# Performance work log

Hardware: AMD Instinct MI355X
Metric: run time of the kernel (lower is better)

## Reference

```python
import jax, jax.numpy as jnp
import numpy as np

B, S, D, H = 2, 2048, 1024, 16
HD = D // H


def setup_inputs() -> dict:
    key = jax.random.key(0)
    ks = jax.random.split(key, 8)
    scale = 1.0 / np.sqrt(D)
    return {
        "x": jax.random.normal(ks[0], (B, S, D), dtype=jnp.float32),
        "y": jax.random.normal(ks[1], (B, S, D), dtype=jnp.float32),
        "gamma": jnp.ones((D,), jnp.float32),
        "beta": jnp.zeros((D,), jnp.float32),
        "in_proj_w": jax.random.uniform(ks[2], (3 * D, D), jnp.float32, -scale, scale),
        "in_proj_b": jnp.zeros((3 * D,), jnp.float32),
        "out_w": jax.random.uniform(ks[3], (D, D), jnp.float32, -scale, scale),
        "out_b": jnp.zeros((D,), jnp.float32),
    }


def _layer_norm(x, gamma, beta, eps=1e-5):
    mu = jnp.mean(x, axis=-1, keepdims=True)
    var = jnp.mean((x - mu) ** 2, axis=-1, keepdims=True)
    return (x - mu) * jax.lax.rsqrt(var + eps) * gamma + beta


def reference(x, y, gamma, beta, in_proj_w, in_proj_b, out_w, out_b):
    # Pre-LN (note: y is unused by the original forward; q=k=v=norm(x))
    xn = _layer_norm(x, gamma, beta)
    # combined QKV projection, PyTorch convention: xn @ W^T + b
    qkv = jnp.einsum("bsd,ed->bse", xn, in_proj_w) + in_proj_b  # (B,S,3D)
    q, k, v = jnp.split(qkv, 3, axis=-1)
    # (B,H,S,HD)
    q = q.reshape(B, S, H, HD).transpose(0, 2, 1, 3)
    k = k.reshape(B, S, H, HD).transpose(0, 2, 1, 3)
    v = v.reshape(B, S, H, HD).transpose(0, 2, 1, 3)
    scores = jnp.einsum("bhqd,bhkd->bhqk", q, k) / np.sqrt(HD)
    attn = jax.nn.softmax(scores, axis=-1)  # (B,H,S,S)
    ctx = jnp.einsum("bhqk,bhkd->bhqd", attn, v)
    ctx = ctx.transpose(0, 2, 1, 3).reshape(B, S, D)
    out = jnp.einsum("bsd,ed->bse", ctx, out_w) + out_b
    # dropout p=0.0 -> identity; residual
    out = out + x
    # average_attn_weights=True default in PyTorch
    attn_w = jnp.mean(attn, axis=1)  # (B,S,S)
    return out, attn_w
```

## Files before the change

### kernel.cpp

```cpp
#include <hip/hip_runtime.h>
#include <hip/hip_bf16.h>

#define Bb 2
#define Ss 2048
#define Dd 1024
#define Hh 16
#define HDd 64
#define Mm (Bb*Ss)
#define N3 (3*Dd)

typedef __attribute__((ext_vector_type(8))) __bf16 bf16x8;
typedef __attribute__((ext_vector_type(4))) float f32x4;
typedef __attribute__((ext_vector_type(16))) float f32x16;
typedef __attribute__((ext_vector_type(8))) short short8;

__device__ __forceinline__ unsigned short f2b(float f) {
  unsigned int u = __float_as_uint(f);
  return (unsigned short)((u + 0x7fffu + ((u >> 16) & 1u)) >> 16);
}

__device__ __forceinline__ f32x4 mfma16(bf16x8 a, bf16x8 b, f32x4 c) {
  return __builtin_amdgcn_mfma_f32_16x16x32_bf16(a, b, c, 0, 0, 0);
}
__device__ __forceinline__ f32x16 mfma32(bf16x8 a, bf16x8 b, f32x16 c) {
  return __builtin_amdgcn_mfma_f32_32x32x16_bf16(a, b, c, 0, 0, 0);
}
__device__ __forceinline__ unsigned cvtpk(float lo, float hi) {
  unsigned r; asm("v_cvt_pk_bf16_f32 %0, %1, %2" : "=v"(r) : "v"(lo), "v"(hi)); return r;
}
__device__ __forceinline__ float fexp2(float x) {
  float r; asm("v_exp_f32 %0, %1" : "=v"(r) : "v"(x)); return r;
}
__device__ __forceinline__ void gload16(const unsigned short* g, unsigned short* l) {
  __builtin_amdgcn_global_load_lds((const __attribute__((address_space(1))) void*)g,
                                   (__attribute__((address_space(3))) void*)l, 16, 0, 0);
}

__global__ __launch_bounds__(256) void ln_kernel(const float* __restrict__ x,
                                                 const float* __restrict__ gamma,
                                                 const float* __restrict__ beta,
                                                 unsigned short* __restrict__ xn) {
  int row = blockIdx.x;
  const float* xr = x + (size_t)row * Dd;
  int t = threadIdx.x;
  float4 v = ((const float4*)xr)[t];
  float s  = v.x + v.y + v.z + v.w;
  float ss = v.x*v.x + v.y*v.y + v.z*v.z + v.w*v.w;
  for (int m = 1; m < 64; m <<= 1) { s += __shfl_xor(s, m, 64); ss += __shfl_xor(ss, m, 64); }
  __shared__ float rs[4], rss[4];
  int w = t >> 6;
  if ((t & 63) == 0) { rs[w] = s; rss[w] = ss; }
  __syncthreads();
  s  = rs[0] + rs[1] + rs[2] + rs[3];
  ss = rss[0] + rss[1] + rss[2] + rss[3];
  float mu   = s * (1.0f / Dd);
  float var  = ss * (1.0f / Dd) - mu * mu;
  float rstd = rsqrtf(var + 1e-5f);
  float4 g  = ((const float4*)gamma)[t];
  float4 be = ((const float4*)beta)[t];
  ushort4 o;
  o.x = f2b((v.x - mu) * rstd * g.x + be.x);
  o.y = f2b((v.y - mu) * rstd * g.y + be.y);
  o.z = f2b((v.z - mu) * rstd * g.z + be.z);
  o.w = f2b((v.w - mu) * rstd * g.w + be.w);
  ((ushort4*)(xn + (size_t)row * Dd))[t] = o;
}

__global__ __launch_bounds__(256) void castw_kernel(const float* __restrict__ w,
                                                    unsigned short* __restrict__ o, int n4) {
  for (int i = blockIdx.x * 256 + threadIdx.x; i < n4; i += gridDim.x * 256) {
    float4 v = ((const float4*)w)[i];
    ushort4 u; u.x = f2b(v.x); u.y = f2b(v.y); u.z = f2b(v.z); u.w = f2b(v.w);
    ((ushort4*)o)[i] = u;
  }
}

__global__ __launch_bounds__(256) void qkv_gemm_kernel(
    const unsigned short* __restrict__ A, const unsigned short* __restrict__ Bw,
    const float* __restrict__ bias,
    unsigned short* __restrict__ qb, unsigned short* __restrict__ kb,
    unsigned short* __restrict__ vtb) {
  __shared__ __align__(16) unsigned short As[64][64];
  __shared__ __align__(16) unsigned short Bs[128][64];
  const int t = threadIdx.x, l = t & 63, w = t >> 6;
  const int wr = w >> 1, wc = w & 1;
  const int lin = blockIdx.x;
  const int swz = (lin & 7) * 192 + (lin >> 3);
  const int mb = (swz & 63) * 64, nb = (swz >> 6) * 128;
  const int sc8 = ((l & 7) ^ ((l >> 3) & 7)) * 8;
  f32x4 acc[2][4];
  for (int i = 0; i < 2; i++) for (int j = 0; j < 4; j++) acc[i][j] = f32x4{0.f,0.f,0.f,0.f};
  for (int kt = 0; kt < 1024; kt += 64) {
    __syncthreads();
#pragma unroll
    for (int j = 0; j < 2; ++j) {
      int rbase = w*16 + j*8;
      gload16(&A[(size_t)(mb + rbase + (l >> 3))*1024 + kt + sc8], &As[rbase][0]);
    }
#pragma unroll
    for (int j = 0; j < 4; ++j) {
      int rbase = w*32 + j*8;
      gload16(&Bw[(size_t)(nb + rbase + (l >> 3))*1024 + kt + sc8], &Bs[rbase][0]);
    }
    __syncthreads();
#pragma unroll
    for (int ks = 0; ks < 2; ++ks) {
      bf16x8 af[2], bfr[4];
      const int g = ks*4 + (l >> 4);
#pragma unroll
      for (int i = 0; i < 2; i++) {
        int row = wr*32 + i*16 + (l & 15);
        af[i] = *(const bf16x8*)&As[row][(g ^ (row & 7))*8];
      }
#pragma unroll
      for (int j = 0; j < 4; j++) {
        int row = wc*64 + j*16 + (l & 15);
        bfr[j] = *(const bf16x8*)&Bs[row][(g ^ (row & 7))*8];
      }
#pragma unroll
      for (int i = 0; i < 2; i++)
#pragma unroll
        for (int j = 0; j < 4; j++)
          acc[i][j] = mfma16(af[i], bfr[j], acc[i][j]);
    }
  }
  const int rbase = (l >> 4) * 4;
#pragma unroll
  for (int i = 0; i < 2; i++) {
#pragma unroll
    for (int j = 0; j < 4; j++) {
      int ncol = nb + wc*64 + j*16 + (l & 15);
      int which = ncol >> 10, d = ncol & 1023, h = d >> 6, hd = d & 63;
      float bv = bias[ncol];
      int mrow0 = mb + wr*32 + i*16 + rbase;
      int b = mrow0 >> 11, s0 = mrow0 & 2047;
      if (which == 2) {
        ushort4 u;
        u.x = f2b(acc[i][j][0] + bv); u.y = f2b(acc[i][j][1] + bv);
        u.z = f2b(acc[i][j][2] + bv); u.w = f2b(acc[i][j][3] + bv);
        *(ushort4*)&vtb[((size_t)(b*Hh + h)*HDd + hd)*Ss + s0] = u;
      } else {
        unsigned short* dst = (which == 0) ? qb : kb;
        float sc = (which == 0) ? 0.18033688f : 1.0f;
#pragma unroll
        for (int r = 0; r < 4; r++)
          dst[((size_t)(b*Hh + h)*Ss + s0 + r)*HDd + hd] = f2b((acc[i][j][r] + bv) * sc);
      }
    }
  }
}

__global__ __launch_bounds__(512) void ctx_kernel(const unsigned short* __restrict__ q,
                                                  const unsigned short* __restrict__ k,
                                                  const unsigned short* __restrict__ vt,
                                                  float* __restrict__ linv,
                                                  unsigned short* __restrict__ ctxb) {
  const int bh = blockIdx.x, qt = blockIdx.y;
  const int b = bh >> 4, h = bh & 15;
  const unsigned short* qp  = q  + (size_t)bh * Ss * HDd;
  const unsigned short* kp  = k  + (size_t)bh * Ss * HDd;
  const unsigned short* vtp = vt + (size_t)bh * HDd * Ss;
  const int t = threadIdx.x, l = t & 63, w = t >> 6;
  const int wq = w & 3, wk = w >> 2;
  const int l31 = l & 31, hi = l >> 5;
  __shared__ __align__(16) unsigned short Ks[2][2][64][64];
  __shared__ __align__(16) unsigned short Vs[2][2][64][64];
  __shared__ float ls[8][32];
  const int qbase = qt*128 + wq*32;
  const int sc8 = ((l & 7) ^ ((l >> 3) & 7)) * 8;
  const int kofs = wk * 1024;
  bf16x8 qfr[4];
#pragma unroll
  for (int c = 0; c < 4; ++c)
    qfr[c] = *(const bf16x8*)&qp[(size_t)(qbase + l31)*HDd + c*16 + hi*8];
#pragma unroll
  for (int j = 0; j < 2; ++j) {
    int rbase = wq*16 + j*8;
    int row = rbase + (l >> 3);
    gload16(&kp [(size_t)(kofs + row)*HDd + sc8], &Ks[wk][0][rbase][0]);
    gload16(&vtp[(size_t)row*Ss + kofs + sc8],    &Vs[wk][0][rbase][0]);
  }
  __syncthreads();

  f32x16 cacc[2];
#pragma unroll
  for (int dj = 0; dj < 2; ++dj)
#pragma unroll
    for (int r = 0; r < 16; ++r) cacc[dj][r] = 0.f;
  float lsum = 0.f;

  for (int it = 0; it < 16; ++it) {
    const int cur = it & 1;
    if (it < 15) {
      int kt = kofs + (it + 1) * 64;
#pragma unroll
      for (int j = 0; j < 2; ++j) {
        int rbase = wq*16 + j*8;
        int row = rbase + (l >> 3);
        gload16(&kp [(size_t)(kt + row)*HDd + sc8], &Ks[wk][cur^1][rbase][0]);
        gload16(&vtp[(size_t)row*Ss + kt + sc8],    &Vs[wk][cur^1][rbase][0]);
      }
    }
#pragma unroll
    for (int kj = 0; kj < 2; ++kj) {
      f32x16 sacc;
#pragma unroll
      for (int r = 0; r < 16; ++r) sacc[r] = 0.f;
      __builtin_amdgcn_s_setprio(1);
#pragma unroll
      for (int c = 0; c < 4; ++c) {
        int R = kj*32 + l31;
        int s = 2*c + hi;
        bf16x8 kf = *(const bf16x8*)&Ks[wk][cur][R][(s ^ (R & 7))*8];
        sacc = mfma32(kf, qfr[c], sacc);
      }
      __builtin_amdgcn_s_setprio(0);
      float p[16];
#pragma unroll
      for (int r = 0; r < 16; ++r) { p[r] = fexp2(sacc[r]); lsum += p[r]; }
      unsigned xa = cvtpk(p[0],p[1]),   xb = cvtpk(p[4],p[5]);
      unsigned ya = cvtpk(p[2],p[3]),   yb = cvtpk(p[6],p[7]);
      unsigned za = cvtpk(p[8],p[9]),   zb = cvtpk(p[12],p[13]);
      unsigned wa = cvtpk(p[10],p[11]), wb = cvtpk(p[14],p[15]);
      asm volatile("v_permlane32_swap_b32 %0, %1" : "+v"(xa), "+v"(xb));
      asm volatile("v_permlane32_swap_b32 %0, %1" : "+v"(ya), "+v"(yb));
      asm volatile("v_permlane32_swap_b32 %0, %1" : "+v"(za), "+v"(zb));
      asm volatile("v_permlane32_swap_b32 %0, %1" : "+v"(wa), "+v"(wb));
      union { unsigned u[4]; bf16x8 v; } f0, f1;
      f0.u[0]=xa; f0.u[1]=ya; f0.u[2]=xb; f0.u[3]=yb;
      f1.u[0]=za; f1.u[1]=wa; f1.u[2]=zb; f1.u[3]=wb;
      __builtin_amdgcn_s_setprio(1);
#pragma unroll
      for (int kc = 0; kc < 2; ++kc) {
        bf16x8 pa = kc ? f1.v : f0.v;
#pragma unroll
        for (int dj = 0; dj < 2; ++dj) {
          int Rv = dj*32 + l31;
          int s = 4*kj + 2*kc + hi;
          bf16x8 vb = *(const bf16x8*)&Vs[wk][cur][Rv][(s ^ (Rv & 7))*8];
          cacc[dj] = mfma32(pa, vb, cacc[dj]);
        }
      }
      __builtin_amdgcn_s_setprio(0);
    }
    __syncthreads();
  }
  lsum += __shfl_xor(lsum, 32, 64);
  if (l < 32) ls[w][l] = lsum;
  float* scr = (float*)&Ks[0][0][0][0];
  if (wk == 1) {
#pragma unroll
    for (int dj = 0; dj < 2; ++dj)
#pragma unroll
      for (int r = 0; r < 16; ++r)
        scr[((wq*2 + dj)*16 + r)*64 + l] = cacc[dj][r];
  }
  __syncthreads();
  if (wk == 0) {
#pragma unroll
    for (int dj = 0; dj < 2; ++dj)
#pragma unroll
      for (int r = 0; r < 16; ++r)
        cacc[dj][r] += scr[((wq*2 + dj)*16 + r)*64 + l];
    if (l < 32) {
      float li = 1.0f / (ls[w][l] + ls[w + 4][l]);
      ls[w][l] = li;
      linv[(size_t)bh*Ss + qbase + l] = li;
    }
    float li4[4][4];
#pragma unroll
    for (int g = 0; g < 4; ++g) {
      f32x4 v4 = *(const f32x4*)&ls[w][8*g + 4*hi];
#pragma unroll
      for (int j = 0; j < 4; ++j) li4[g][j] = v4[j];
    }
#pragma unroll
    for (int dj = 0; dj < 2; ++dj) {
      int d = h*64 + dj*32 + l31;
#pragma unroll
      for (int r = 0; r < 16; ++r) {
        int qq = qbase + (r & 3) + 8*(r >> 2) + 4*hi;
        ctxb[((size_t)b*Ss + qq)*Dd + d] = f2b(cacc[dj][r] * li4[r >> 2][r & 3]);
      }
    }
  }
}

__global__ __launch_bounds__(256) void attnw_kernel(const unsigned short* __restrict__ q,
                                                    const unsigned short* __restrict__ k,
                                                    const float* __restrict__ linv,
                                                    float* __restrict__ attw) {
  const int lin = blockIdx.x;
  const int xcd = lin & 7, j0 = lin >> 3;
  const int ktile = (xcd & 3)*8 + (j0 & 7);
  const int qt    = (xcd >> 2)*8 + ((j0 >> 3) & 7);
  const int b     = j0 >> 6;
  const int t = threadIdx.x, l = t & 63, w = t >> 6;
  const int l31 = l & 31, hi = l >> 5;
  __shared__ union __align__(16) {
    struct { unsigned short qbuf[128][64]; unsigned short kbuf[64][64]; } g;
    float ps[128][68];
  } L;
  const int qbase = qt*128 + w*32;
  const int qrow = qbase + l31;
  const int sc8 = ((l & 7) ^ ((l >> 3) & 7)) * 8;

  float psum[2][16];
#pragma unroll
  for (int kj = 0; kj < 2; ++kj)
#pragma unroll
    for (int r = 0; r < 16; ++r) psum[kj][r] = 0.f;

#pragma unroll 1
  for (int h = 0; h < 16; ++h) {
    __syncthreads();
    const unsigned short* qp = q + ((size_t)(b*Hh + h)*Ss + (size_t)qt*128)*HDd;
    const unsigned short* kp = k + ((size_t)(b*Hh + h)*Ss + (size_t)ktile*64)*HDd;
#pragma unroll
    for (int j = 0; j < 4; ++j) {
      int rbase = w*32 + j*8;
      gload16(&qp[(size_t)(rbase + (l >> 3))*HDd + sc8], &L.g.qbuf[rbase][0]);
    }
#pragma unroll
    for (int j = 0; j < 2; ++j) {
      int rbase = w*16 + j*8;
      gload16(&kp[(size_t)(rbase + (l >> 3))*HDd + sc8], &L.g.kbuf[rbase][0]);
    }
    float li = linv[(size_t)(b*Hh + h)*Ss + qrow];
    __syncthreads();
    bf16x8 qfr[4];
#pragma unroll
    for (int c = 0; c < 4; ++c) {
      int row = w*32 + l31;
      int s = 2*c + hi;
      qfr[c] = *(const bf16x8*)&L.g.qbuf[row][(s ^ (row & 7))*8];
    }
#pragma unroll
    for (int kj = 0; kj < 2; ++kj) {
      f32x16 sacc;
#pragma unroll
      for (int r = 0; r < 16; ++r) sacc[r] = 0.f;
      __builtin_amdgcn_s_setprio(1);
#pragma unroll
      for (int c = 0; c < 4; ++c) {
        int R = kj*32 + l31;
        int s = 2*c + hi;
        bf16x8 kf = *(const bf16x8*)&L.g.kbuf[R][(s ^ (R & 7))*8];
        sacc = mfma32(kf, qfr[c], sacc);
      }
      __builtin_amdgcn_s_setprio(0);
#pragma unroll
      for (int r = 0; r < 16; ++r) psum[kj][r] += fexp2(sacc[r]) * li;
    }
  }

  __syncthreads();
#pragma unroll
  for (int kj = 0; kj < 2; ++kj)
#pragma unroll
    for (int r = 0; r < 16; ++r) {
      int krow = kj*32 + (r & 3) + 8*(r >> 2) + 4*hi;
      L.ps[w*32 + l31][krow] = psum[kj][r] * (1.0f/16.0f);
    }
  __syncthreads();
#pragma unroll
  for (int pass = 0; pass < 8; ++pass) {
    int row = pass*16 + (t >> 4), c4 = (t & 15) * 4;
    float4 v = *(const float4*)&L.ps[row][c4];
    *(float4*)&attw[((size_t)b*Ss + qt*128 + row)*Ss + (size_t)ktile*64 + c4] = v;
  }
}

__global__ __launch_bounds__(256) void out_gemm_kernel(
    const unsigned short* __restrict__ A, const unsigned short* __restrict__ Bw,
    const float* __restrict__ bias, const float* __restrict__ x,
    float* __restrict__ outp) {
  __shared__ __align__(16) unsigned short As[128][64];
  __shared__ __align__(16) unsigned short Bs[64][64];
  const int t = threadIdx.x, l = t & 63, w = t >> 6;
  const int wr = w >> 1, wc = w & 1;
  const int mb = blockIdx.x * 128, nb = blockIdx.y * 64;
  const int sc8 = ((l & 7) ^ ((l >> 3) & 7)) * 8;
  f32x4 acc[4][2];
  for (int i = 0; i < 4; i++) for (int j = 0; j < 2; j++) acc[i][j] = f32x4{0.f,0.f,0.f,0.f};
  for (int kt = 0; kt < 1024; kt += 64) {
    __syncthreads();
#pragma unroll
    for (int j = 0; j < 4; ++j) {
      int rbase = w*32 + j*8;
      int row = rbase + (l >> 3);
      gload16(&A[(size_t)(mb + row)*1024 + kt + sc8], &As[rbase][0]);
    }
#pragma unroll
    for (int j = 0; j < 2; ++j) {
      int rbase = w*16 + j*8;
      int row = rbase + (l >> 3);
      gload16(&Bw[(size_t)(nb + row)*1024 + kt + sc8], &Bs[rbase][0]);
    }
    __syncthreads();
#pragma unroll
    for (int ks = 0; ks < 2; ++ks) {
      bf16x8 af[4], bfr[2];
      const int g = ks*4 + (l >> 4);
#pragma unroll
      for (int i = 0; i < 4; i++) {
        int row = wr*64 + i*16 + (l & 15);
        af[i] = *(const bf16x8*)&As[row][(g ^ (row & 7))*8];
      }
#pragma unroll
      for (int j = 0; j < 2; j++) {
        int row = wc*32 + j*16 + (l & 15);
        bfr[j] = *(const bf16x8*)&Bs[row][(g ^ (row & 7))*8];
      }
#pragma unroll
      for (int i = 0; i < 4; i++)
#pragma unroll
        for (int j = 0; j < 2; j++)
          acc[i][j] = mfma16(af[i], bfr[j], acc[i][j]);
    }
  }
  const int rbase = (l >> 4) * 4;
#pragma unroll
  for (int i = 0; i < 4; i++) {
#pragma unroll
    for (int j = 0; j < 2; j++) {
      int ncol = nb + wc*32 + j*16 + (l & 15);
      float bv = bias[ncol];
#pragma unroll
      for (int r = 0; r < 4; r++) {
        int mrow = mb + wr*64 + i*16 + rbase + r;
        size_t idx = (size_t)mrow * 1024 + ncol;
        outp[idx] = acc[i][j][r] + bv + x[idx];
      }
    }
  }
}

extern "C" void kernel_launch(void* const* d_in, const int* in_sizes, int n_in,
                              void* d_out, int out_size, void* d_ws, size_t ws_size,
                              hipStream_t stream) {
  const float* x     = (const float*)d_in[0];
  const float* gamma = (const float*)d_in[2];
  const float* beta  = (const float*)d_in[3];
  const float* w_in  = (const float*)d_in[4];
  const float* b_in  = (const float*)d_in[5];
  const float* w_out = (const float*)d_in[6];
  const float* b_out = (const float*)d_in[7];
  float* outp = (float*)d_out;
  float* attw = outp + (size_t)Mm * Dd;

  char* ws = (char*)d_ws;
  unsigned short* xn   = (unsigned short*)(ws + 0);
  unsigned short* wqkv = (unsigned short*)(ws + 8388608);
  unsigned short* wout = (unsigned short*)(ws + 14680064);
  unsigned short* qb   = (unsigned short*)(ws + 16777216);
  unsigned short* kb   = (unsigned short*)(ws + 25165824);
  unsigned short* vtb  = (unsigned short*)(ws + 33554432);
  float*          linv = (float*)(ws + 41943040);
  unsigned short* ctxb = (unsigned short*)(ws + 42205184);

  ln_kernel<<<Mm, 256, 0, stream>>>(x, gamma, beta, xn);
  castw_kernel<<<1024, 256, 0, stream>>>(w_in, wqkv, (N3 * Dd) / 4);
  castw_kernel<<<512, 256, 0, stream>>>(w_out, wout, (Dd * Dd) / 4);
  qkv_gemm_kernel<<<(Mm/64)*(N3/128), 256, 0, stream>>>(xn, wqkv, b_in, qb, kb, vtb);
  ctx_kernel<<<dim3(Bb*Hh, Ss/128), 512, 0, stream>>>(qb, kb, vtb, linv, ctxb);
  attnw_kernel<<<1024, 256, 0, stream>>>(qb, kb, linv, attw);
  out_gemm_kernel<<<dim3(Mm/128, Dd/64), 256, 0, stream>>>(ctxb, wout, b_out, x, outp);
}
```

Measured before the change: 143.7 us.

## Merge prep kernels and run attention-weight and output GEMM blocks in one launch

Merges layer norm and the two weight casts into a single prep kernel that dispatches on block index, removing two launches. Also merges the attention-weight averaging kernel and the output projection GEMM into one launch, interleaving them two attnw blocks to one GEMM block so the independent GEMM work can overlap the bandwidth-heavy attnw stores. The cost is a larger shared-memory union and a heavier register footprint in the combined kernels, which may reduce occupancy for the lighter branch.

```diff
diff --git a/kernel.cpp b/kernel.cpp
--- a/kernel.cpp
+++ b/kernel.cpp
@@ -36,42 +36,52 @@
                                    (__attribute__((address_space(3))) void*)l, 16, 0, 0);
 }
 
-__global__ __launch_bounds__(256) void ln_kernel(const float* __restrict__ x,
-                                                 const float* __restrict__ gamma,
-                                                 const float* __restrict__ beta,
-                                                 unsigned short* __restrict__ xn) {
-  int row = blockIdx.x;
-  const float* xr = x + (size_t)row * Dd;
-  int t = threadIdx.x;
-  float4 v = ((const float4*)xr)[t];
-  float s  = v.x + v.y + v.z + v.w;
-  float ss = v.x*v.x + v.y*v.y + v.z*v.z + v.w*v.w;
-  for (int m = 1; m < 64; m <<= 1) { s += __shfl_xor(s, m, 64); ss += __shfl_xor(ss, m, 64); }
-  __shared__ float rs[4], rss[4];
-  int w = t >> 6;
-  if ((t & 63) == 0) { rs[w] = s; rss[w] = ss; }
-  __syncthreads();
-  s  = rs[0] + rs[1] + rs[2] + rs[3];
-  ss = rss[0] + rss[1] + rss[2] + rss[3];
-  float mu   = s * (1.0f / Dd);
-  float var  = ss * (1.0f / Dd) - mu * mu;
-  float rstd = rsqrtf(var + 1e-5f);
-  float4 g  = ((const float4*)gamma)[t];
-  float4 be = ((const float4*)beta)[t];
-  ushort4 o;
-  o.x = f2b((v.x - mu) * rstd * g.x + be.x);
-  o.y = f2b((v.y - mu) * rstd * g.y + be.y);
-  o.z = f2b((v.z - mu) * rstd * g.z + be.z);
-  o.w = f2b((v.w - mu) * rstd * g.w + be.w);
-  ((ushort4*)(xn + (size_t)row * Dd))[t] = o;
-}
-
-__global__ __launch_bounds__(256) void castw_kernel(const float* __restrict__ w,
-                                                    unsigned short* __restrict__ o, int n4) {
-  for (int i = blockIdx.x * 256 + threadIdx.x; i < n4; i += gridDim.x * 256) {
-    float4 v = ((const float4*)w)[i];
-    ushort4 u; u.x = f2b(v.x); u.y = f2b(v.y); u.z = f2b(v.z); u.w = f2b(v.w);
-    ((ushort4*)o)[i] = u;
+__global__ __launch_bounds__(256) void prep_kernel(const float* __restrict__ x,
+                                                   const float* __restrict__ gamma,
+                                                   const float* __restrict__ beta,
+                                                   unsigned short* __restrict__ xn,
+                                                   const float* __restrict__ w_in,
+                                                   unsigned short* __restrict__ wqkv,
+                                                   const float* __restrict__ w_out,
+                                                   unsigned short* __restrict__ wout) {
+  const int bid = blockIdx.x, t = threadIdx.x;
+  if (bid < Mm) {
+    const float* xr = x + (size_t)bid * Dd;
+    float4 v = ((const float4*)xr)[t];
+    float s  = v.x + v.y + v.z + v.w;
+    float ss = v.x*v.x + v.y*v.y + v.z*v.z + v.w*v.w;
+    for (int m = 1; m < 64; m <<= 1) { s += __shfl_xor(s, m, 64); ss += __shfl_xor(ss, m, 64); }
+    __shared__ float rs[4], rss[4];
+    int w = t >> 6;
+    if ((t & 63) == 0) { rs[w] = s; rss[w] = ss; }
+    __syncthreads();
+    s  = rs[0] + rs[1] + rs[2] + rs[3];
+    ss = rss[0] + rss[1] + rss[2] + rss[3];
+    float mu   = s * (1.0f / Dd);
+    float var  = ss * (1.0f / Dd) - mu * mu;
+    float rstd = rsqrtf(var + 1e-5f);
+    float4 g  = ((const float4*)gamma)[t];
+    float4 be = ((const float4*)beta)[t];
+    ushort4 o;
+    o.x = f2b((v.x - mu) * rstd * g.x + be.x);
+    o.y = f2b((v.y - mu) * rstd * g.y + be.y);
+    o.z = f2b((v.z - mu) * rstd * g.z + be.z);
+    o.w = f2b((v.w - mu) * rstd * g.w + be.w);
+    ((ushort4*)(xn + (size_t)bid * Dd))[t] = o;
+  } else if (bid < Mm + 1024) {
+    const int b2 = bid - Mm;
+    for (int i = b2*256 + t; i < (N3*Dd)/4; i += 1024*256) {
+      float4 v = ((const float4*)w_in)[i];
+      ushort4 u; u.x = f2b(v.x); u.y = f2b(v.y); u.z = f2b(v.z); u.w = f2b(v.w);
+      ((ushort4*)wqkv)[i] = u;
+    }
+  } else {
+    const int b2 = bid - Mm - 1024;
+    for (int i = b2*256 + t; i < (Dd*Dd)/4; i += 512*256) {
+      float4 v = ((const float4*)w_out)[i];
+      ushort4 u; u.x = f2b(v.x); u.y = f2b(v.y); u.z = f2b(v.z); u.w = f2b(v.w);
+      ((ushort4*)wout)[i] = u;
+    }
   }
 }
 
@@ -286,151 +296,150 @@
   }
 }
 
-__global__ __launch_bounds__(256) void attnw_kernel(const unsigned short* __restrict__ q,
-                                                    const unsigned short* __restrict__ k,
-                                                    const float* __restrict__ linv,
-                                                    float* __restrict__ attw) {
-  const int lin = blockIdx.x;
-  const int xcd = lin & 7, j0 = lin >> 3;
-  const int ktile = (xcd & 3)*8 + (j0 & 7);
-  const int qt    = (xcd >> 2)*8 + ((j0 >> 3) & 7);
-  const int b     = j0 >> 6;
-  const int t = threadIdx.x, l = t & 63, w = t >> 6;
-  const int l31 = l & 31, hi = l >> 5;
+__global__ __launch_bounds__(256) void attnw_out_kernel(
+    const unsigned short* __restrict__ q, const unsigned short* __restrict__ k,
+    const float* __restrict__ linv, float* __restrict__ attw,
+    const unsigned short* __restrict__ ctxb, const unsigned short* __restrict__ wout,
+    const float* __restrict__ bias, const float* __restrict__ x,
+    float* __restrict__ outp) {
   __shared__ union __align__(16) {
     struct { unsigned short qbuf[128][64]; unsigned short kbuf[64][64]; } g;
     float ps[128][68];
+    struct { unsigned short As[128][64]; unsigned short Bs[64][64]; } o;
   } L;
-  const int qbase = qt*128 + w*32;
-  const int qrow = qbase + l31;
-  const int sc8 = ((l & 7) ^ ((l >> 3) & 7)) * 8;
-
-  float psum[2][16];
-#pragma unroll
-  for (int kj = 0; kj < 2; ++kj)
-#pragma unroll
-    for (int r = 0; r < 16; ++r) psum[kj][r] = 0.f;
+  const int t = threadIdx.x, l = t & 63, w = t >> 6;
+  const int r3 = blockIdx.x % 3;
+  if (r3 < 2) {
+    const int lin = (blockIdx.x / 3) * 2 + r3;
+    const int xcd = lin & 7, j0 = lin >> 3;
+    const int ktile = (xcd & 3)*8 + (j0 & 7);
+    const int qt    = (xcd >> 2)*8 + ((j0 >> 3) & 7);
+    const int b     = j0 >> 6;
+    const int l31 = l & 31, hi = l >> 5;
+    const int qbase = qt*128 + w*32;
+    const int qrow = qbase + l31;
+    const int sc8 = ((l & 7) ^ ((l >> 3) & 7)) * 8;
+
+    float psum[2][16];
+#pragma unroll
+    for (int kj = 0; kj < 2; ++kj)
+#pragma unroll
+      for (int r = 0; r < 16; ++r) psum[kj][r] = 0.f;
 
 #pragma unroll 1
-  for (int h = 0; h < 16; ++h) {
-    __syncthreads();
-    const unsigned short* qp = q + ((size_t)(b*Hh + h)*Ss + (size_t)qt*128)*HDd;
-    const unsigned short* kp = k + ((size_t)(b*Hh + h)*Ss + (size_t)ktile*64)*HDd;
-#pragma unroll
-    for (int j = 0; j < 4; ++j) {
-      int rbase = w*32 + j*8;
-      gload16(&qp[(size_t)(rbase + (l >> 3))*HDd + sc8], &L.g.qbuf[rbase][0]);
-    }
-#pragma unroll
-    for (int j = 0; j < 2; ++j) {
-      int rbase = w*16 + j*8;
-      gload16(&kp[(size_t)(rbase + (l >> 3))*HDd + sc8], &L.g.kbuf[rbase][0]);
-    }
-    float li = linv[(size_t)(b*Hh + h)*Ss + qrow];
-    __syncthreads();
-    bf16x8 qfr[4];
-#pragma unroll
-    for (int c = 0; c < 4; ++c) {
-      int row = w*32 + l31;
-      int s = 2*c + hi;
-      qfr[c] = *(const bf16x8*)&L.g.qbuf[row][(s ^ (row & 7))*8];
-    }
-#pragma unroll
-    for (int kj = 0; kj < 2; ++kj) {
-      f32x16 sacc;
-#pragma unroll
-      for (int r = 0; r < 16; ++r) sacc[r] = 0.f;
-      __builtin_amdgcn_s_setprio(1);
+    for (int h = 0; h < 16; ++h) {
+      __syncthreads();
+      const unsigned short* qp = q + ((size_t)(b*Hh + h)*Ss + (size_t)qt*128)*HDd;
+      const unsigned short* kp = k + ((size_t)(b*Hh + h)*Ss + (size_t)ktile*64)*HDd;
+#pragma unroll
+      for (int j = 0; j < 4; ++j) {
+        int rbase = w*32 + j*8;
+        gload16(&qp[(size_t)(rbase + (l >> 3))*HDd + sc8], &L.g.qbuf[rbase][0]);
+      }
+#pragma unroll
+      for (int j = 0; j < 2; ++j) {
+        int rbase = w*16 + j*8;
+        gload16(&kp[(size_t)(rbase + (l >> 3))*HDd + sc8], &L.g.kbuf[rbase][0]);
+      }
+      float li = linv[(size_t)(b*Hh + h)*Ss + qrow];
+      __syncthreads();
+      bf16x8 qfr[4];
 #pragma unroll
       for (int c = 0; c < 4; ++c) {
-        int R = kj*32 + l31;
+        int row = w*32 + l31;
         int s = 2*c + hi;
-        bf16x8 kf = *(const bf16x8*)&L.g.kbuf[R][(s ^ (R & 7))*8];
-        sacc = mfma32(kf, qfr[c], sacc);
-      }
-      __builtin_amdgcn_s_setprio(0);
-#pragma unroll
-      for (int r = 0; r < 16; ++r) psum[kj][r] += fexp2(sacc[r]) * li;
-    }
-  }
-
-  __syncthreads();
-#pragma unroll
-  for (int kj = 0; kj < 2; ++kj)
-#pragma unroll
-    for (int r = 0; r < 16; ++r) {
-      int krow = kj*32 + (r & 3) + 8*(r >> 2) + 4*hi;
-      L.ps[w*32 + l31][krow] = psum[kj][r] * (1.0f/16.0f);
-    }
-  __syncthreads();
-#pragma unroll
-  for (int pass = 0; pass < 8; ++pass) {
-    int row = pass*16 + (t >> 4), c4 = (t & 15) * 4;
-    float4 v = *(const float4*)&L.ps[row][c4];
-    *(float4*)&attw[((size_t)b*Ss + qt*128 + row)*Ss + (size_t)ktile*64 + c4] = v;
-  }
-}
-
-__global__ __launch_bounds__(256) void out_gemm_kernel(
-    const unsigned short* __restrict__ A, const unsigned short* __restrict__ Bw,
-    const float* __restrict__ bias, const float* __restrict__ x,
-    float* __restrict__ outp) {
-  __shared__ __align__(16) unsigned short As[128][64];
-  __shared__ __align__(16) unsigned short Bs[64][64];
-  const int t = threadIdx.x, l = t & 63, w = t >> 6;
-  const int wr = w >> 1, wc = w & 1;
-  const int mb = blockIdx.x * 128, nb = blockIdx.y * 64;
-  const int sc8 = ((l & 7) ^ ((l >> 3) & 7)) * 8;
-  f32x4 acc[4][2];
-  for (int i = 0; i < 4; i++) for (int j = 0; j < 2; j++) acc[i][j] = f32x4{0.f,0.f,0.f,0.f};
-  for (int kt = 0; kt < 1024; kt += 64) {
-    __syncthreads();
-#pragma unroll
-    for (int j = 0; j < 4; ++j) {
-      int rbase = w*32 + j*8;
-      int row = rbase + (l >> 3);
-      gload16(&A[(size_t)(mb + row)*1024 + kt + sc8], &As[rbase][0]);
-    }
-#pragma unroll
-    for (int j = 0; j < 2; ++j) {
-      int rbase = w*16 + j*8;
-      int row = rbase + (l >> 3);
-      gload16(&Bw[(size_t)(nb + row)*1024 + kt + sc8], &Bs[rbase][0]);
-    }
-    __syncthreads();
-#pragma unroll
-    for (int ks = 0; ks < 2; ++ks) {
-      bf16x8 af[4], bfr[2];
-      const int g = ks*4 + (l >> 4);
-#pragma unroll
-      for (int i = 0; i < 4; i++) {
-        int row = wr*64 + i*16 + (l & 15);
-        af[i] = *(const bf16x8*)&As[row][(g ^ (row & 7))*8];
-      }
+        qfr[c] = *(const bf16x8*)&L.g.qbuf[row][(s ^ (row & 7))*8];
+      }
+#pragma unroll
+      for (int kj = 0; kj < 2; ++kj) {
+        f32x16 sacc;
+#pragma unroll
+        for (int r = 0; r < 16; ++r) sacc[r] = 0.f;
+        __builtin_amdgcn_s_setprio(1);
+#pragma unroll
+        for (int c = 0; c < 4; ++c) {
+          int R = kj*32 + l31;
+          int s = 2*c + hi;
+          bf16x8 kf = *(const bf16x8*)&L.g.kbuf[R][(s ^ (R & 7))*8];
+          sacc = mfma32(kf, qfr[c], sacc);
+        }
+        __builtin_amdgcn_s_setprio(0);
+#pragma unroll
+        for (int r = 0; r < 16; ++r) psum[kj][r] += fexp2(sacc[r]) * li;
+      }
+    }
+
+    __syncthreads();
+#pragma unroll
+    for (int kj = 0; kj < 2; ++kj)
+#pragma unroll
+      for (int r = 0; r < 16; ++r) {
+        int krow = kj*32 + (r & 3) + 8*(r >> 2) + 4*hi;
+        L.ps[w*32 + l31][krow] = psum[kj][r] * (1.0f/16.0f);
+      }
+    __syncthreads();
+#pragma unroll
+    for (int pass = 0; pass < 8; ++pass) {
+      int row = pass*16 + (t >> 4), c4 = (t & 15) * 4;
+      float4 v = *(const float4*)&L.ps[row][c4];
+      *(float4*)&attw[((size_t)b*Ss + qt*128 + row)*Ss + (size_t)ktile*64 + c4] = v;
+    }
+  } else {
+    const int ob = blockIdx.x / 3;
+    const int wr = w >> 1, wc = w & 1;
+    const int mb = (ob & 31) * 128, nb = (ob >> 5) * 64;
+    const int sc8 = ((l & 7) ^ ((l >> 3) & 7)) * 8;
+    f32x4 acc[4][2];
+    for (int i = 0; i < 4; i++) for (int j = 0; j < 2; j++) acc[i][j] = f32x4{0.f,0.f,0.f,0.f};
+    for (int kt = 0; kt < 1024; kt += 64) {
+      __syncthreads();
+#pragma unroll
+      for (int j = 0; j < 4; ++j) {
+        int rbase = w*32 + j*8;
+        int row = rbase + (l >> 3);
+        gload16(&ctxb[(size_t)(mb + row)*1024 + kt + sc8], &L.o.As[rbase][0]);
+      }
+#pragma unroll
+      for (int j = 0; j < 2; ++j) {
+        int rbase = w*16 + j*8;
+        int row = rbase + (l >> 3);
+        gload16(&wout[(size_t)(nb + row)*1024 + kt + sc8], &L.o.Bs[rbase][0]);
+      }
+      __syncthreads();
+#pragma unroll
+      for (int ks = 0; ks < 2; ++ks) {
+        bf16x8 af[4], bfr[2];
+        const int g = ks*4 + (l >> 4);
+#pragma unroll
+        for (int i = 0; i < 4; i++) {
+          int row = wr*64 + i*16 + (l & 15);
+          af[i] = *(const bf16x8*)&L.o.As[row][(g ^ (row & 7))*8];
+        }
+#pragma unroll
+        for (int j = 0; j < 2; j++) {
+          int row = wc*32 + j*16 + (l & 15);
+          bfr[j] = *(const bf16x8*)&L.o.Bs[row][(g ^ (row & 7))*8];
+        }
+#pragma unroll
+        for (int i = 0; i < 4; i++)
+#pragma unroll
+          for (int j = 0; j < 2; j++)
+            acc[i][j] = mfma16(af[i], bfr[j], acc[i][j]);
+      }
+    }
+    const int rbase = (l >> 4) * 4;
+#pragma unroll
+    for (int i = 0; i < 4; i++) {
 #pragma unroll
       for (int j = 0; j < 2; j++) {
-        int row = wc*32 + j*16 + (l & 15);
-        bfr[j] = *(const bf16x8*)&Bs[row][(g ^ (row & 7))*8];
-      }
-#pragma unroll
-      for (int i = 0; i < 4; i++)
-#pragma unroll
-        for (int j = 0; j < 2; j++)
-          acc[i][j] = mfma16(af[i], bfr[j], acc[i][j]);
-    }
-  }
-  const int rbase = (l >> 4) * 4;
-#pragma unroll
-  for (int i = 0; i < 4; i++) {
-#pragma unroll
-    for (int j = 0; j < 2; j++) {
-      int ncol = nb + wc*32 + j*16 + (l & 15);
-      float bv = bias[ncol];
-#pragma unroll
-      for (int r = 0; r < 4; r++) {
-        int mrow = mb + wr*64 + i*16 + rbase + r;
-        size_t idx = (size_t)mrow * 1024 + ncol;
-        outp[idx] = acc[i][j][r] + bv + x[idx];
+        int ncol = nb + wc*32 + j*16 + (l & 15);
+        float bv = bias[ncol];
+#pragma unroll
+        for (int r = 0; r < 4; r++) {
+          int mrow = mb + wr*64 + i*16 + rbase + r;
+          size_t idx = (size_t)mrow * 1024 + ncol;
+          outp[idx] = acc[i][j][r] + bv + x[idx];
+        }
       }
     }
   }
@@ -459,11 +468,8 @@
   float*          linv = (float*)(ws + 41943040);
   unsigned short* ctxb = (unsigned short*)(ws + 42205184);
 
-  ln_kernel<<<Mm, 256, 0, stream>>>(x, gamma, beta, xn);
-  castw_kernel<<<1024, 256, 0, stream>>>(w_in, wqkv, (N3 * Dd) / 4);
-  castw_kernel<<<512, 256, 0, stream>>>(w_out, wout, (Dd * Dd) / 4);
+  prep_kernel<<<Mm + 1024 + 512, 256, 0, stream>>>(x, gamma, beta, xn, w_in, wqkv, w_out, wout);
   qkv_gemm_kernel<<<(Mm/64)*(N3/128), 256, 0, stream>>>(xn, wqkv, b_in, qb, kb, vtb);
   ctx_kernel<<<dim3(Bb*Hh, Ss/128), 512, 0, stream>>>(qb, kb, vtb, linv, ctxb);
-  attnw_kernel<<<1024, 256, 0, stream>>>(qb, kb, linv, attw);
-  out_gemm_kernel<<<dim3(Mm/128, Dd/64), 256, 0, stream>>>(ctxb, wout, b_out, x, outp);
-}
+  attnw_out_kernel<<<1536, 256, 0, stream>>>(qb, kb, linv, attw, ctxb, wout, b_out, x, outp);
+}
```

Result: faster. 136.9 us, median of 2 (-4.7%).
